# Performance work log

Hardware: AMD Instinct MI355X
Metric: run time of the kernel (lower is better)

Reference implementation:

```python
import jax, jax.numpy as jnp
import numpy as np

LN_EPS = 1e-5


def setup_inputs() -> dict:
    key = jax.random.key(0)
    ks = jax.random.split(key, 10)
    b, n, m, d, e = 2, 4096, 32, 128, 64
    return {
        "t_ij": jax.random.normal(ks[0], (b, n, m, d), dtype=jnp.float32),
        "x1": jax.random.normal(ks[1], (b, n, d, 3), dtype=jnp.float32),
        "x2": jax.random.normal(ks[2], (b, n, d, 5), dtype=jnp.float32),
        "neighbor_indices": jax.random.randint(ks[3], (b, n, m), 0, n),
        "to_queries": jax.random.normal(ks[4], (d, e), dtype=jnp.float32),
        "to_keys1": jax.random.normal(ks[5], (d, e), dtype=jnp.float32),
        "to_keys2": jax.random.normal(ks[6], (d, e), dtype=jnp.float32),
        "ln_weight": jnp.ones((2 * e,), dtype=jnp.float32),
        "edge_w": jax.random.normal(ks[7], (2 * e, d), dtype=jnp.float32) / np.sqrt(2 * e),
        "res_w": jax.random.normal(ks[8], (d, d), dtype=jnp.float32) / np.sqrt(d),
    }


def _degree_inner_product(xl, to_queries, to_keys, neighbor_indices):
    # xl: [b n d ml]; projections over channel dim d -> e
    q = jnp.einsum('bndm,de->bnem', xl, to_queries)   # [b n e ml]
    k = jnp.einsum('bndm,de->bnem', xl, to_keys)      # [b n e ml]
    # gather neighbor keys: [b n j e ml]
    kg = jax.vmap(lambda kk, idx: kk[idx])(k, neighbor_indices)
    # inner product over multiplicity ml, per feature e: [b n j e]
    return jnp.einsum('bnem,bnjem->bnje', q, kg)


def reference(t_ij, x1, x2, neighbor_indices, to_queries, to_keys1, to_keys2,
              ln_weight, edge_w, res_w):
    ip1 = _degree_inner_product(x1, to_queries, to_keys1, neighbor_indices)
    ip2 = _degree_inner_product(x2, to_queries, to_keys2, neighbor_indices)
    w_ij = jnp.concatenate([ip1, ip2], axis=-1)  # [b n j 2e]
    # LayerNorm over last dim, weight only (bias=False)
    mu = jnp.mean(w_ij, axis=-1, keepdims=True)
    var = jnp.mean((w_ij - mu) ** 2, axis=-1, keepdims=True)
    w_ij = (w_ij - mu) * jax.lax.rsqrt(var + LN_EPS) * ln_weight
    edge_out = jax.nn.sigmoid(jnp.einsum('bnje,ed->bnjd', w_ij, edge_w))
    res_out = jnp.einsum('bnjd,de->bnje', t_ij, res_w)
    return edge_out + res_out
```

## Files before the change

kernel.cpp:

```cpp
#include <hip/hip_runtime.h>

#define B_ 2
#define N_ 4096
#define M_ 32
#define D_ 128
#define E_ 64
#define LN_EPS 1e-5f
#define WST 136
#define TOT (B_ * N_)
#define FGRID 512

typedef __bf16 bf16x8 __attribute__((ext_vector_type(8)));
typedef float  f32x4  __attribute__((ext_vector_type(4)));

__global__ __launch_bounds__(256) void proj_kernel(
    const float* __restrict__ x1, const float* __restrict__ x2,
    const float* __restrict__ Wq, const float* __restrict__ Wk1,
    const float* __restrict__ Wk2,
    float* __restrict__ qws, __bf16* __restrict__ kws)
{
    __shared__ float xs[4][D_ * 8];
    const int lane = threadIdx.x & 63;
    const int wv   = threadIdx.x >> 6;
    const int bn   = blockIdx.x * 4 + wv;
    float* xw = xs[wv];
    const float* __restrict__ x1p = x1 + (size_t)bn * (D_ * 3);
    const float* __restrict__ x2p = x2 + (size_t)bn * (D_ * 5);
    for (int i = lane; i < D_ * 3; i += 64) xw[(i / 3) * 8 + (i % 3)]     = x1p[i];
    for (int i = lane; i < D_ * 5; i += 64) xw[(i / 5) * 8 + 3 + (i % 5)] = x2p[i];
    __syncthreads();

    float q[8] = {0.f,0.f,0.f,0.f,0.f,0.f,0.f,0.f};
    float k[8] = {0.f,0.f,0.f,0.f,0.f,0.f,0.f,0.f};
    #pragma unroll 4
    for (int d = 0; d < D_; ++d) {
        const float4 xa = *(const float4*)&xw[d * 8];
        const float4 xb = *(const float4*)&xw[d * 8 + 4];
        const float wq  = Wq [d * E_ + lane];
        const float wk1 = Wk1[d * E_ + lane];
        const float wk2 = Wk2[d * E_ + lane];
        q[0] += xa.x * wq;  q[1] += xa.y * wq;  q[2] += xa.z * wq;  q[3] += xa.w * wq;
        q[4] += xb.x * wq;  q[5] += xb.y * wq;  q[6] += xb.z * wq;  q[7] += xb.w * wq;
        k[0] += xa.x * wk1; k[1] += xa.y * wk1; k[2] += xa.z * wk1;
        k[3] += xa.w * wk2; k[4] += xb.x * wk2; k[5] += xb.y * wk2;
        k[6] += xb.z * wk2; k[7] += xb.w * wk2;
    }
    float4* qo = (float4*)(qws + ((size_t)bn * E_ + lane) * 8);
    qo[0] = make_float4(q[0], q[1], q[2], q[3]);
    qo[1] = make_float4(q[4], q[5], q[6], q[7]);
    bf16x8 kb;
    #pragma unroll
    for (int s = 0; s < 8; ++s) kb[s] = (__bf16)k[s];
    *(bf16x8*)(kws + ((size_t)bn * E_ + lane) * 8) = kb;
}

__global__ __launch_bounds__(512, 4) void fused_kernel(
    const float* __restrict__ t_ij, const int* __restrict__ nidx,
    const float* __restrict__ qws, const __bf16* __restrict__ kws,
    const float* __restrict__ ln_w,
    const float* __restrict__ edge_w, const float* __restrict__ res_w,
    float* __restrict__ out)
{
    __shared__ __bf16 wbuf[3][M_ * WST];

    const int t    = threadIdx.x;
    const int lane = t & 63;
    const int wvu  = t >> 6;
    const int r16  = lane & 15;
    const int quad = lane >> 4;
    const int n0   = wvu * 16;

    bf16x8 bE[4], bR[4];
    #pragma unroll
    for (int ks = 0; ks < 4; ++ks) {
        const int k0 = ks * 32 + quad * 8;
        bf16x8 fe, fr;
        #pragma unroll
        for (int j = 0; j < 8; ++j) {
            fe[j] = (__bf16)edge_w[(k0 + j) * D_ + n0 + r16];
            fr[j] = (__bf16)res_w [(k0 + j) * D_ + n0 + r16];
        }
        bE[ks] = fe;
        bR[ks] = fr;
    }

    const float lnlo = ln_w[lane];
    const float lnhi = ln_w[64 + lane];
    const int stride = gridDim.x;

    int    ni[4];
    bf16x8 kv[4];
    float4 qa, qb;
    bf16x8 tf[8];

    auto nidxLoad = [&](int bn) {
        const int* np = nidx + (size_t)bn * M_ + wvu * 4;
        #pragma unroll
        for (int jj = 0; jj < 4; ++jj) ni[jj] = np[jj];
    };
    auto gatherIssue = [&](int bn) {
        const int b = bn >> 12;
        #pragma unroll
        for (int jj = 0; jj < 4; ++jj)
            kv[jj] = *(const bf16x8*)&kws[((size_t)(b * N_ + ni[jj]) * E_ + lane) * 8];
        const float* qp = qws + ((size_t)bn * E_ + lane) * 8;
        qa = *(const float4*)qp;
        qb = *(const float4*)(qp + 4);
    };

    auto phaseW = [&](__bf16* buf) {
        #pragma unroll
        for (int jj = 0; jj < 4; ++jj) {
            const int j = wvu * 4 + jj;
            const bf16x8 k8 = kv[jj];
            const float wlo = qa.x * (float)k8[0] + qa.y * (float)k8[1]
                            + qa.z * (float)k8[2];
            const float whi = qa.w * (float)k8[3] + qb.x * (float)k8[4]
                            + qb.y * (float)k8[5] + qb.z * (float)k8[6]
                            + qb.w * (float)k8[7];
            float s1 = wlo + whi;
            float s2 = wlo * wlo + whi * whi;
            #pragma unroll
            for (int off = 1; off < 64; off <<= 1) {
                s1 += __shfl_xor(s1, off, 64);
                s2 += __shfl_xor(s2, off, 64);
            }
            const float mu  = s1 * (1.f / 128.f);
            const float var = fmaxf(s2 * (1.f / 128.f) - mu * mu, 0.f);
            const float rs  = rsqrtf(var + LN_EPS);
            buf[j * WST + lane]      = (__bf16)((wlo - mu) * rs * lnlo);
            buf[j * WST + 64 + lane] = (__bf16)((whi - mu) * rs * lnhi);
        }
    };

    auto tload = [&](int bn) {
        const float* tp = t_ij + ((size_t)bn * M_) * D_;
        #pragma unroll
        for (int mt = 0; mt < 2; ++mt) {
            const float* tpr = tp + (size_t)(mt * 16 + r16) * D_;
            #pragma unroll
            for (int ks = 0; ks < 4; ++ks) {
                const int ko = ks * 32 + quad * 8;
                const float4 t0 = *(const float4*)(tpr + ko);
                const float4 t1 = *(const float4*)(tpr + ko + 4);
                bf16x8 a;
                a[0]=(__bf16)t0.x; a[1]=(__bf16)t0.y; a[2]=(__bf16)t0.z; a[3]=(__bf16)t0.w;
                a[4]=(__bf16)t1.x; a[5]=(__bf16)t1.y; a[6]=(__bf16)t1.z; a[7]=(__bf16)t1.w;
                tf[mt * 4 + ks] = a;
            }
        }
    };

    auto phaseM = [&](int bn, const __bf16* buf) {
        const size_t jb = (size_t)bn * M_;
        f32x4 accE[2], accR[2];
        #pragma unroll
        for (int mt = 0; mt < 2; ++mt) {
            accE[mt] = (f32x4){0.f,0.f,0.f,0.f};
            accR[mt] = (f32x4){0.f,0.f,0.f,0.f};
        }
        #pragma unroll
        for (int ks = 0; ks < 4; ++ks) {
            const bf16x8 aW0 = *(const bf16x8*)&buf[r16 * WST + ks * 32 + quad * 8];
            const bf16x8 aW1 = *(const bf16x8*)&buf[(16 + r16) * WST + ks * 32 + quad * 8];
            accE[0] = __builtin_amdgcn_mfma_f32_16x16x32_bf16(aW0,      bE[ks], accE[0], 0, 0, 0);
            accR[0] = __builtin_amdgcn_mfma_f32_16x16x32_bf16(tf[ks],   bR[ks], accR[0], 0, 0, 0);
            accE[1] = __builtin_amdgcn_mfma_f32_16x16x32_bf16(aW1,      bE[ks], accE[1], 0, 0, 0);
            accR[1] = __builtin_amdgcn_mfma_f32_16x16x32_bf16(tf[4+ks], bR[ks], accR[1], 0, 0, 0);
        }
        #pragma unroll
        for (int mt = 0; mt < 2; ++mt)
            #pragma unroll
            for (int rr = 0; rr < 4; ++rr) {
                const int row = mt * 16 + quad * 4 + rr;
                const float e  = accE[mt][rr];
                const float sg = 1.f / (1.f + __expf(-e));
                out[(jb + row) * D_ + n0 + r16] = sg + accR[mt][rr];
            }
    };

    const int bn0 = blockIdx.x;
    auto cb = [](int x) { return x < TOT ? x : TOT - 1; };

    nidxLoad(bn0);
    gatherIssue(bn0);
    nidxLoad(cb(bn0 + stride));
    phaseW(wbuf[0]);
    gatherIssue(cb(bn0 + stride));
    nidxLoad(cb(bn0 + 2 * stride));
    tload(bn0);

    int buf = 0;
    for (int bn = bn0; bn < TOT; bn += stride) {
        const int nbuf = (buf == 2) ? 0 : buf + 1;
        phaseW(wbuf[nbuf]);
        __syncthreads();
        phaseM(bn, wbuf[buf]);
        gatherIssue(cb(bn + 2 * stride));
        nidxLoad(cb(bn + 3 * stride));
        tload(cb(bn + stride));
        buf = nbuf;
    }
}

extern "C" void kernel_launch(void* const* d_in, const int* in_sizes, int n_in,
                              void* d_out, int out_size, void* d_ws, size_t ws_size,
                              hipStream_t stream) {
    const float* t_ij = (const float*)d_in[0];
    const float* x1   = (const float*)d_in[1];
    const float* x2   = (const float*)d_in[2];
    const int*   nidx = (const int*)  d_in[3];
    const float* Wq   = (const float*)d_in[4];
    const float* Wk1  = (const float*)d_in[5];
    const float* Wk2  = (const float*)d_in[6];
    const float* lnw  = (const float*)d_in[7];
    const float* eww  = (const float*)d_in[8];
    const float* rww  = (const float*)d_in[9];
    float* out = (float*)d_out;

    float*  qws = (float*)d_ws;
    __bf16* kws = (__bf16*)(qws + (size_t)TOT * E_ * 8);

    proj_kernel<<<TOT / 4, 256, 0, stream>>>(x1, x2, Wq, Wk1, Wk2, qws, kws);
    fused_kernel<<<FGRID, 512, 0, stream>>>(t_ij, nidx, qws, kws, lnw, eww, rww, out);
}
```

Before: 414.6 us.

## Widen per-wave output tile to 32 columns and halve block size

Each wave of the fused kernel now computes two 16-column output tiles over 8 neighbor rows, using 4 waves per 256-thread block instead of 8 waves per 512-thread block. This halves the number of waves that each redundantly load and convert the full t_ij tile and the gathered keys per item. The grid grows to 768 blocks, and the next gather is issued before the MFMA phase to overlap its latency. In exchange each wave holds twice as many weight fragments and accumulators in registers, which can lower occupancy.

```diff
diff --git a/kernel.cpp b/kernel.cpp
--- a/kernel.cpp
+++ b/kernel.cpp
@@ -8,7 +8,6 @@
 #define LN_EPS 1e-5f
 #define WST 136
 #define TOT (B_ * N_)
-#define FGRID 512
 
 typedef __bf16 bf16x8 __attribute__((ext_vector_type(8)));
 typedef float  f32x4  __attribute__((ext_vector_type(4)));
@@ -54,7 +53,7 @@
     *(bf16x8*)(kws + ((size_t)bn * E_ + lane) * 8) = kb;
 }
 
-__global__ __launch_bounds__(512, 4) void fused_kernel(
+__global__ __launch_bounds__(256, 3) void fused_kernel(
     const float* __restrict__ t_ij, const int* __restrict__ nidx,
     const float* __restrict__ qws, const __bf16* __restrict__ kws,
     const float* __restrict__ ln_w,
@@ -68,40 +67,44 @@
     const int wvu  = t >> 6;
     const int r16  = lane & 15;
     const int quad = lane >> 4;
-    const int n0   = wvu * 16;
-
-    bf16x8 bE[4], bR[4];
+    const int n0   = wvu * 32;
+
+    bf16x8 bE[2][4], bR[2][4];
     #pragma unroll
-    for (int ks = 0; ks < 4; ++ks) {
-        const int k0 = ks * 32 + quad * 8;
-        bf16x8 fe, fr;
-        #pragma unroll
-        for (int j = 0; j < 8; ++j) {
-            fe[j] = (__bf16)edge_w[(k0 + j) * D_ + n0 + r16];
-            fr[j] = (__bf16)res_w [(k0 + j) * D_ + n0 + r16];
-        }
-        bE[ks] = fe;
-        bR[ks] = fr;
+    for (int nt = 0; nt < 2; ++nt) {
+        const int col = n0 + nt * 16 + r16;
+        #pragma unroll
+        for (int ks = 0; ks < 4; ++ks) {
+            const int k0 = ks * 32 + quad * 8;
+            bf16x8 fe, fr;
+            #pragma unroll
+            for (int j = 0; j < 8; ++j) {
+                fe[j] = (__bf16)edge_w[(k0 + j) * D_ + col];
+                fr[j] = (__bf16)res_w [(k0 + j) * D_ + col];
+            }
+            bE[nt][ks] = fe;
+            bR[nt][ks] = fr;
+        }
     }
 
     const float lnlo = ln_w[lane];
     const float lnhi = ln_w[64 + lane];
     const int stride = gridDim.x;
 
-    int    ni[4];
-    bf16x8 kv[4];
+    int    ni[8];
+    bf16x8 kv[8];
     float4 qa, qb;
     bf16x8 tf[8];
 
     auto nidxLoad = [&](int bn) {
-        const int* np = nidx + (size_t)bn * M_ + wvu * 4;
-        #pragma unroll
-        for (int jj = 0; jj < 4; ++jj) ni[jj] = np[jj];
+        const size_t jb = (size_t)bn * M_ + wvu * 8;
+        #pragma unroll
+        for (int jj = 0; jj < 8; ++jj) ni[jj] = nidx[jb + jj];
     };
     auto gatherIssue = [&](int bn) {
         const int b = bn >> 12;
         #pragma unroll
-        for (int jj = 0; jj < 4; ++jj)
+        for (int jj = 0; jj < 8; ++jj)
             kv[jj] = *(const bf16x8*)&kws[((size_t)(b * N_ + ni[jj]) * E_ + lane) * 8];
         const float* qp = qws + ((size_t)bn * E_ + lane) * 8;
         qa = *(const float4*)qp;
@@ -110,8 +113,8 @@
 
     auto phaseW = [&](__bf16* buf) {
         #pragma unroll
-        for (int jj = 0; jj < 4; ++jj) {
-            const int j = wvu * 4 + jj;
+        for (int jj = 0; jj < 8; ++jj) {
+            const int j  = wvu * 8 + jj;
             const bf16x8 k8 = kv[jj];
             const float wlo = qa.x * (float)k8[0] + qa.y * (float)k8[1]
                             + qa.z * (float)k8[2];
@@ -153,30 +156,38 @@
 
     auto phaseM = [&](int bn, const __bf16* buf) {
         const size_t jb = (size_t)bn * M_;
-        f32x4 accE[2], accR[2];
-        #pragma unroll
-        for (int mt = 0; mt < 2; ++mt) {
-            accE[mt] = (f32x4){0.f,0.f,0.f,0.f};
-            accR[mt] = (f32x4){0.f,0.f,0.f,0.f};
-        }
+        f32x4 accE[2][2], accR[2][2];
+        #pragma unroll
+        for (int mt = 0; mt < 2; ++mt)
+            #pragma unroll
+            for (int nt = 0; nt < 2; ++nt) {
+                accE[mt][nt] = (f32x4){0.f,0.f,0.f,0.f};
+                accR[mt][nt] = (f32x4){0.f,0.f,0.f,0.f};
+            }
         #pragma unroll
         for (int ks = 0; ks < 4; ++ks) {
             const bf16x8 aW0 = *(const bf16x8*)&buf[r16 * WST + ks * 32 + quad * 8];
             const bf16x8 aW1 = *(const bf16x8*)&buf[(16 + r16) * WST + ks * 32 + quad * 8];
-            accE[0] = __builtin_amdgcn_mfma_f32_16x16x32_bf16(aW0,      bE[ks], accE[0], 0, 0, 0);
-            accR[0] = __builtin_amdgcn_mfma_f32_16x16x32_bf16(tf[ks],   bR[ks], accR[0], 0, 0, 0);
-            accE[1] = __builtin_amdgcn_mfma_f32_16x16x32_bf16(aW1,      bE[ks], accE[1], 0, 0, 0);
-            accR[1] = __builtin_amdgcn_mfma_f32_16x16x32_bf16(tf[4+ks], bR[ks], accR[1], 0, 0, 0);
+            #pragma unroll
+            for (int nt = 0; nt < 2; ++nt) {
+                accE[0][nt] = __builtin_amdgcn_mfma_f32_16x16x32_bf16(aW0,      bE[nt][ks], accE[0][nt], 0, 0, 0);
+                accR[0][nt] = __builtin_amdgcn_mfma_f32_16x16x32_bf16(tf[ks],   bR[nt][ks], accR[0][nt], 0, 0, 0);
+                accE[1][nt] = __builtin_amdgcn_mfma_f32_16x16x32_bf16(aW1,      bE[nt][ks], accE[1][nt], 0, 0, 0);
+                accR[1][nt] = __builtin_amdgcn_mfma_f32_16x16x32_bf16(tf[4+ks], bR[nt][ks], accR[1][nt], 0, 0, 0);
+            }
         }
         #pragma unroll
         for (int mt = 0; mt < 2; ++mt)
             #pragma unroll
-            for (int rr = 0; rr < 4; ++rr) {
-                const int row = mt * 16 + quad * 4 + rr;
-                const float e  = accE[mt][rr];
-                const float sg = 1.f / (1.f + __expf(-e));
-                out[(jb + row) * D_ + n0 + r16] = sg + accR[mt][rr];
-            }
+            for (int nt = 0; nt < 2; ++nt)
+                #pragma unroll
+                for (int rr = 0; rr < 4; ++rr) {
+                    const int row = mt * 16 + quad * 4 + rr;
+                    const int col = n0 + nt * 16 + r16;
+                    const float e  = accE[mt][nt][rr];
+                    const float sg = 1.f / (1.f + __expf(-e));
+                    out[(jb + row) * D_ + col] = sg + accR[mt][nt][rr];
+                }
     };
 
     const int bn0 = blockIdx.x;
@@ -195,10 +206,10 @@
         const int nbuf = (buf == 2) ? 0 : buf + 1;
         phaseW(wbuf[nbuf]);
         __syncthreads();
+        gatherIssue(cb(bn + 2 * stride));
         phaseM(bn, wbuf[buf]);
-        gatherIssue(cb(bn + 2 * stride));
+        tload(cb(bn + stride));
         nidxLoad(cb(bn + 3 * stride));
-        tload(cb(bn + stride));
         buf = nbuf;
     }
 }
@@ -222,5 +233,5 @@
     __bf16* kws = (__bf16*)(qws + (size_t)TOT * E_ * 8);
 
     proj_kernel<<<TOT / 4, 256, 0, stream>>>(x1, x2, Wq, Wk1, Wk2, qws, kws);
-    fused_kernel<<<FGRID, 512, 0, stream>>>(t_ij, nidx, qws, kws, lnw, eww, rww, out);
+    fused_kernel<<<768, 256, 0, stream>>>(t_ij, nidx, qws, kws, lnw, eww, rww, out);
 }
```

New measurement: 422.3 us. About the same (+1.9%).
